# Performance work log

Measured on AMD Instinct MI355X. Metric: run time of the kernel, lower is better.

Reference implementation:

```python
import jax, jax.numpy as jnp
import numpy as np

H, W = 512, 512  # image_size from init_kwargs


def _render_single(xyz, color, opacity):
    """Faithful JAX version of GaussianRenderer._fallback_render (the path the
    module executes when the CUDA rasterizer is unavailable), vectorized.
    Point-splat each Gaussian to one pixel, depth-sort descending (back-to-front),
    alpha-composite: a_k = o_k * prod_{j<k}(1 - o_j); depth = z of front-most hit.
    xyz: (N,3)  color: (N,3)  opacity: (N,1)
    """
    N = xyz.shape[0]
    focal = (H + W) / 2.0
    z = xyz[:, 2]
    xf = xyz[:, 0] / (z + 1e-6) * focal + W / 2.0
    yf = xyz[:, 1] / (z + 1e-6) * focal + H / 2.0
    # torch .long() truncates toward zero
    xi = jnp.trunc(jnp.clip(xf, -1e9, 1e9)).astype(jnp.int32)
    yi = jnp.trunc(jnp.clip(yf, -1e9, 1e9)).astype(jnp.int32)
    valid = (xi >= 0) & (xi < W) & (yi >= 0) & (yi < H)
    pix = jnp.where(valid, yi * W + xi, H * W)  # dummy slot H*W for out-of-bounds
    # stable sort: primary pixel ascending, secondary z descending (back-to-front)
    order = jnp.lexsort((-z, pix))
    pix_s, z_s = pix[order], z[order]
    o_s = opacity[order, 0]
    c_s = color[order]
    valid_s = pix_s < H * W
    # per-pixel exclusive transmittance: alpha recurrence 1-A_k = (1-A_{k-1})(1-o_k)
    logt = jnp.log(jnp.clip(1.0 - o_s, 1e-12, None))
    cs = jnp.cumsum(logt)
    excl = cs - logt  # exclusive cumsum (global)
    start = jnp.concatenate([jnp.ones((1,), bool), pix_s[1:] != pix_s[:-1]])
    start_idx = jax.lax.cummax(jnp.where(start, jnp.arange(N), -1))
    T_prev = jnp.exp(excl - excl[start_idx])  # exclusive within pixel segment
    a = jnp.where(valid_s, o_s * T_prev, 0.0)
    img = jnp.zeros((H * W + 1, 3), xyz.dtype).at[pix_s].add(a[:, None] * c_s)
    # depth: last element written per pixel (front-most, smallest z in segment)
    end = jnp.concatenate([pix_s[1:] != pix_s[:-1], jnp.ones((1,), bool)])
    dpix = jnp.where(end & valid_s, pix_s, H * W)
    depth = jnp.zeros((H * W + 1,), xyz.dtype).at[dpix].set(z_s)
    render = img[: H * W].reshape(H, W, 3).transpose(2, 0, 1)  # (3,H,W)
    return render, depth[: H * W].reshape(1, H, W)


def setup_inputs() -> dict:
    key = jax.random.key(0)
    ks = jax.random.split(key, 5)
    B, N = 8, 262144
    return {
        "xyz": jax.random.normal(ks[0], (B, N, 3), jnp.float32),
        "scale": jax.random.normal(ks[1], (B, N, 3), jnp.float32),
        "rotation": jax.random.normal(ks[2], (B, N, 1), jnp.float32),
        "opacity": jax.random.uniform(ks[3], (B, N, 1), jnp.float32),
        "color": jax.random.uniform(ks[4], (B, N, 3), jnp.float32),
    }


def reference(xyz, scale, rotation, opacity, color):
    # scale/rotation are accepted (part of the gaussians dict) but unused by the
    # fallback renderer, matching the torch source.
    render, depth = jax.vmap(_render_single)(xyz, color, opacity)
    return render, depth
```

## Files before the change

kernel.cpp:

```cpp
#include <hip/hip_runtime.h>
#include <stdint.h>

#define W_ 512
#define H_ 512
#define HW_ (512 * 512)
#define RMAX 4
#define OVF_CAP 65536

__device__ __forceinline__ int project_pix(float x, float y, float z) {
    float zz = z + 1e-6f;
    float xf = x / zz * 512.0f + 256.0f;
    float yf = y / zz * 512.0f + 256.0f;
    xf = fminf(fmaxf(xf, -1e9f), 1e9f);
    yf = fminf(fmaxf(yf, -1e9f), 1e9f);
    int xi = (int)xf;
    int yi = (int)yf;
    if (xi >= 0 && xi < W_ && yi >= 0 && yi < H_) return yi * W_ + xi;
    return -1;
}

__device__ __forceinline__ unsigned int q8(float v) {
    v = fminf(fmaxf(v, 0.f), 1.f);
    return (unsigned int)__float2uint_rn(v * 255.0f);
}
__device__ __forceinline__ float d8(unsigned int u) {
    return (float)(u & 255u) * (1.0f / 255.0f);
}

__global__ void __launch_bounds__(256) k_init(uint4* __restrict__ p, int n4) {
    int i = blockIdx.x * blockDim.x + threadIdx.x;
    if (i < n4) p[i] = make_uint4(0u, 0u, 0u, 0u);
}

__global__ void __launch_bounds__(256) k_build(const float4* __restrict__ xyz4,
                                               const float4* __restrict__ op4,
                                               const float4* __restrict__ col4,
                                               unsigned int* __restrict__ cnt,
                                               unsigned long long* __restrict__ slots,
                                               unsigned int* __restrict__ ovf_hdr,
                                               unsigned int* __restrict__ ovf_pix,
                                               unsigned long long* __restrict__ ovf_rec,
                                               int N, int total4) {
    int t = blockIdx.x * blockDim.x + threadIdx.x;
    if (t >= total4) return;
    float4 v0 = xyz4[3 * (size_t)t + 0];
    float4 v1 = xyz4[3 * (size_t)t + 1];
    float4 v2 = xyz4[3 * (size_t)t + 2];
    float4 o4 = op4[t];
    float4 c0 = col4[3 * (size_t)t + 0];
    float4 c1 = col4[3 * (size_t)t + 1];
    float4 c2 = col4[3 * (size_t)t + 2];
    float xs[4] = {v0.x, v0.w, v1.z, v2.y};
    float ys[4] = {v0.y, v1.x, v1.w, v2.z};
    float zs[4] = {v0.z, v1.y, v2.x, v2.w};
    float os[4] = {o4.x, o4.y, o4.z, o4.w};
    float cr[4] = {c0.x, c0.w, c1.z, c2.y};
    float cg[4] = {c0.y, c1.x, c1.w, c2.z};
    float cb[4] = {c0.z, c1.y, c2.x, c2.w};
    int g0 = 4 * t;
    size_t pbase = (size_t)(g0 / N) * HW_;

    int pix[4];
    unsigned long long rec[4];
#pragma unroll
    for (int j = 0; j < 4; ++j) {
        pix[j] = project_pix(xs[j], ys[j], zs[j]);
        unsigned int pay = q8(os[j]) | (q8(cr[j]) << 8) | (q8(cg[j]) << 16) |
                           (q8(cb[j]) << 24);
        rec[j] = ((unsigned long long)__float_as_uint(zs[j]) << 32) |
                 (unsigned long long)pay;
    }

    size_t p[4];
    unsigned int sh[4], old[4];
#pragma unroll
    for (int j = 0; j < 4; ++j) {
        p[j] = pbase + (pix[j] >= 0 ? pix[j] : 0);
        sh[j] = 16u * (unsigned int)(p[j] & 1);
        if (pix[j] >= 0) old[j] = atomicAdd(&cnt[p[j] >> 1], 1u << sh[j]);
    }

#pragma unroll
    for (int j = 0; j < 4; ++j) {
        if (pix[j] >= 0) {
            unsigned int s = (old[j] >> sh[j]) & 0xffffu;
            if (s < RMAX) {
                slots[p[j] * RMAX + s] = rec[j];
            } else {
                unsigned int i = atomicAdd(ovf_hdr, 1u);
                if (i < OVF_CAP) { ovf_pix[i] = (unsigned int)p[j]; ovf_rec[i] = rec[j]; }
            }
        }
    }
}

__global__ void __launch_bounds__(256) k_composite(const unsigned int* __restrict__ cnt,
                                                   const unsigned long long* __restrict__ slots,
                                                   const unsigned int* __restrict__ ovf_hdr,
                                                   const unsigned int* __restrict__ ovf_pix,
                                                   const unsigned long long* __restrict__ ovf_rec,
                                                   float* __restrict__ out, int B) {
    int q = blockIdx.x * blockDim.x + threadIdx.x;
    int nb8 = B * (HW_ / 8);
    if (q >= nb8) return;
    int p0 = 8 * q;
    int b = p0 / HW_;
    int pl0 = p0 - b * HW_;

    uint4 cw = ((const uint4*)cnt)[q];
    unsigned int ws[4] = {cw.x, cw.y, cw.z, cw.w};

    float rr[8], gg[8], bb[8], dd[8];

#pragma unroll
    for (int j = 0; j < 8; ++j) {
        unsigned int k = (ws[j >> 1] >> (16 * (j & 1))) & 0xffffu;
        float r = 0.f, g2 = 0.f, bl = 0.f, depth = 0.f;
        if (k > 0) {
            size_t p = (size_t)p0 + j;
            const uint4* sp = (const uint4*)&slots[p * RMAX];
            uint4 s01 = sp[0];

            unsigned int pay0 = s01.x;
            float o0 = d8(pay0);
            r  = o0 * d8(pay0 >> 8);
            g2 = o0 * d8(pay0 >> 16);
            bl = o0 * d8(pay0 >> 24);
            depth = __uint_as_float(s01.y);

            if (k >= 2) {
                unsigned int pf = s01.x, pn = s01.z;
                float zf = __uint_as_float(s01.y), zn = __uint_as_float(s01.w);
                bool sw = (zn > zf) || (zn == zf && pn < pf);
                if (sw) {
                    unsigned int tp = pf; pf = pn; pn = tp;
                    float tz = zf; zf = zn; zn = tz;
                }
                float of = d8(pf), on = d8(pn);
                float a1 = on * (1.0f - of);
                r  = of * d8(pf >> 8)  + a1 * d8(pn >> 8);
                g2 = of * d8(pf >> 16) + a1 * d8(pn >> 16);
                bl = of * d8(pf >> 24) + a1 * d8(pn >> 24);
                depth = zn;

                if (k >= 3) {
                    uint4 s23 = sp[1];
                    if (k <= RMAX) {
                        float z_[4];
                        unsigned int y_[4];
                        z_[0] = __uint_as_float(s01.y); y_[0] = s01.x;
                        z_[1] = __uint_as_float(s01.w); y_[1] = s01.z;
                        z_[2] = __uint_as_float(s23.y); y_[2] = s23.x;
                        z_[3] = (k > 3) ? __uint_as_float(s23.w) : -__builtin_inff();
                        y_[3] = s23.z;
#define CE(I, J)                                                                    \
                        {                                                           \
                            bool sw2 = (z_[J] > z_[I]) || (z_[J] == z_[I] && y_[J] < y_[I]); \
                            if (sw2) {                                              \
                                float tz = z_[I]; z_[I] = z_[J]; z_[J] = tz;        \
                                unsigned int ty = y_[I]; y_[I] = y_[J]; y_[J] = ty; \
                            }                                                       \
                        }
                        CE(0,1) CE(2,3) CE(0,2) CE(1,3) CE(1,2)
#undef CE
                        float T = 1.f;
                        r = 0.f; g2 = 0.f; bl = 0.f; depth = 0.f;
#pragma unroll
                        for (int s = 0; s < RMAX; ++s) {
                            if (s < (int)k) {
                                unsigned int pay = y_[s];
                                float o = d8(pay);
                                float a = o * T;
                                r  += a * d8(pay >> 8);
                                g2 += a * d8(pay >> 16);
                                bl += a * d8(pay >> 24);
                                T *= (1.0f - o);
                                depth = z_[s];
                            }
                        }
                    } else {
                        unsigned int nov = ovf_hdr[0];
                        if (nov > OVF_CAP) nov = OVF_CAP;
                        unsigned int ptag = (unsigned int)p;
                        float zz0 = __uint_as_float(s01.y), zz1 = __uint_as_float(s01.w);
                        float zz2 = __uint_as_float(s23.y), zz3 = __uint_as_float(s23.w);
                        float prev_z = __builtin_inff();
                        unsigned int prev_y = 0u;
                        float T = 1.f;
                        r = 0.f; g2 = 0.f; bl = 0.f; depth = 0.f;
                        for (int s = 0; s < (int)k; ++s) {
                            float best_z = -__builtin_inff();
                            unsigned int best_y = ~0u;
#define CAND(Z, Y)                                                                       \
                            {                                                            \
                                float z = (Z); unsigned int y = (Y);                     \
                                bool after  = (z < prev_z) || (z == prev_z && y > prev_y); \
                                bool better = (z > best_z) || (z == best_z && y < best_y); \
                                if (after && better) { best_z = z; best_y = y; }         \
                            }
                            CAND(zz0, s01.x) CAND(zz1, s01.z) CAND(zz2, s23.x) CAND(zz3, s23.z)
                            for (unsigned int t2 = 0; t2 < nov; ++t2) {
                                if (ovf_pix[t2] == ptag) {
                                    unsigned long long rec = ovf_rec[t2];
                                    CAND(__uint_as_float((unsigned int)(rec >> 32)),
                                         (unsigned int)rec)
                                }
                            }
#undef CAND
                            unsigned int pay = best_y;
                            float o = d8(pay);
                            float a = o * T;
                            r  += a * d8(pay >> 8);
                            g2 += a * d8(pay >> 16);
                            bl += a * d8(pay >> 24);
                            T *= (1.0f - o);
                            depth = best_z;
                            prev_z = best_z;
                            prev_y = best_y;
                        }
                    }
                }
            }
        }
        rr[j] = r; gg[j] = g2; bb[j] = bl; dd[j] = depth;
    }

    size_t HWs = (size_t)HW_;
    float* oR = out + ((size_t)b * 3 + 0) * HWs + pl0;
    float* oG = out + ((size_t)b * 3 + 1) * HWs + pl0;
    float* oB = out + ((size_t)b * 3 + 2) * HWs + pl0;
    float* oD = out + (size_t)B * 3 * HWs + (size_t)b * HWs + pl0;
    *(float4*)(oR)     = make_float4(rr[0], rr[1], rr[2], rr[3]);
    *(float4*)(oR + 4) = make_float4(rr[4], rr[5], rr[6], rr[7]);
    *(float4*)(oG)     = make_float4(gg[0], gg[1], gg[2], gg[3]);
    *(float4*)(oG + 4) = make_float4(gg[4], gg[5], gg[6], gg[7]);
    *(float4*)(oB)     = make_float4(bb[0], bb[1], bb[2], bb[3]);
    *(float4*)(oB + 4) = make_float4(bb[4], bb[5], bb[6], bb[7]);
    *(float4*)(oD)     = make_float4(dd[0], dd[1], dd[2], dd[3]);
    *(float4*)(oD + 4) = make_float4(dd[4], dd[5], dd[6], dd[7]);
}

extern "C" void kernel_launch(void* const* d_in, const int* in_sizes, int n_in,
                              void* d_out, int out_size, void* d_ws, size_t ws_size,
                              hipStream_t stream) {
    const float* xyz     = (const float*)d_in[0];
    const float* opacity = (const float*)d_in[3];
    const float* color   = (const float*)d_in[4];
    float* out = (float*)d_out;

    int B = out_size / (4 * HW_);
    int N = in_sizes[0] / (3 * B);
    int total = B * N;
    int nb = B * HW_;

    unsigned int* cnt      = (unsigned int*)d_ws;
    unsigned int* ovf_hdr  = cnt + nb / 2;
    unsigned int* ovf_pix  = ovf_hdr + 64;
    unsigned long long* ovf_rec = (unsigned long long*)(ovf_pix + OVF_CAP);
    unsigned long long* slots   = ovf_rec + OVF_CAP;

    int blk = 256;
    int zwords = nb / 2 + 64;
    int z4 = zwords / 4;
    k_init<<<(z4 + blk - 1) / blk, blk, 0, stream>>>((uint4*)cnt, z4);

    int total4 = total / 4;
    k_build<<<(total4 + blk - 1) / blk, blk, 0, stream>>>((const float4*)xyz,
                                                          (const float4*)opacity,
                                                          (const float4*)color,
                                                          cnt, slots, ovf_hdr, ovf_pix, ovf_rec,
                                                          N, total4);

    int nb8 = nb / 8;
    k_composite<<<(nb8 + blk - 1) / blk, blk, 0, stream>>>(cnt, slots, ovf_hdr, ovf_pix,
                                                           ovf_rec, out, B);
}
```

Baseline: 41.71 us.

## Split per-pixel slot array into dense first-slot plane plus overflow slots

The per-pixel record storage changes from a single 4-slot array to a dense array holding each pixel's first record, plus a separate 3-slot array for the second through fourth. The composite kernel now loads the first records of 8 consecutive pixels with coalesced 16-byte loads and reads the extra slots only for pixels with two or more hits. The build kernel is also restructured to do projection, atomic, and store per point in one loop. The aim is to cut wasted memory traffic, since most pixels hold at most one splat. The cost is a less regular access pattern for multi-hit pixels and the scattered 3-wide layout.

```diff
diff --git a/kernel.cpp b/kernel.cpp
--- a/kernel.cpp
+++ b/kernel.cpp
@@ -36,7 +36,8 @@
                                                const float4* __restrict__ op4,
                                                const float4* __restrict__ col4,
                                                unsigned int* __restrict__ cnt,
-                                               unsigned long long* __restrict__ slots,
+                                               unsigned long long* __restrict__ s0,
+                                               unsigned long long* __restrict__ sx,
                                                unsigned int* __restrict__ ovf_hdr,
                                                unsigned int* __restrict__ ovf_pix,
                                                unsigned long long* __restrict__ ovf_rec,
@@ -59,43 +60,33 @@
     float cb[4] = {c0.z, c1.y, c2.x, c2.w};
     int g0 = 4 * t;
     size_t pbase = (size_t)(g0 / N) * HW_;
-
-    int pix[4];
-    unsigned long long rec[4];
 #pragma unroll
     for (int j = 0; j < 4; ++j) {
-        pix[j] = project_pix(xs[j], ys[j], zs[j]);
-        unsigned int pay = q8(os[j]) | (q8(cr[j]) << 8) | (q8(cg[j]) << 16) |
-                           (q8(cb[j]) << 24);
-        rec[j] = ((unsigned long long)__float_as_uint(zs[j]) << 32) |
-                 (unsigned long long)pay;
-    }
-
-    size_t p[4];
-    unsigned int sh[4], old[4];
-#pragma unroll
-    for (int j = 0; j < 4; ++j) {
-        p[j] = pbase + (pix[j] >= 0 ? pix[j] : 0);
-        sh[j] = 16u * (unsigned int)(p[j] & 1);
-        if (pix[j] >= 0) old[j] = atomicAdd(&cnt[p[j] >> 1], 1u << sh[j]);
-    }
-
-#pragma unroll
-    for (int j = 0; j < 4; ++j) {
-        if (pix[j] >= 0) {
-            unsigned int s = (old[j] >> sh[j]) & 0xffffu;
-            if (s < RMAX) {
-                slots[p[j] * RMAX + s] = rec[j];
+        int pix = project_pix(xs[j], ys[j], zs[j]);
+        if (pix >= 0) {
+            size_t p = pbase + pix;
+            unsigned int sh = 16u * (unsigned int)(p & 1);
+            unsigned int old = atomicAdd(&cnt[p >> 1], 1u << sh);
+            unsigned int s = (old >> sh) & 0xffffu;
+            unsigned int pay = q8(os[j]) | (q8(cr[j]) << 8) | (q8(cg[j]) << 16) |
+                               (q8(cb[j]) << 24);
+            unsigned long long rec =
+                ((unsigned long long)__float_as_uint(zs[j]) << 32) | (unsigned long long)pay;
+            if (s == 0) {
+                s0[p] = rec;
+            } else if (s < RMAX) {
+                sx[p * 3 + (s - 1)] = rec;
             } else {
                 unsigned int i = atomicAdd(ovf_hdr, 1u);
-                if (i < OVF_CAP) { ovf_pix[i] = (unsigned int)p[j]; ovf_rec[i] = rec[j]; }
+                if (i < OVF_CAP) { ovf_pix[i] = (unsigned int)p; ovf_rec[i] = rec; }
             }
         }
     }
 }
 
 __global__ void __launch_bounds__(256) k_composite(const unsigned int* __restrict__ cnt,
-                                                   const unsigned long long* __restrict__ slots,
+                                                   const unsigned long long* __restrict__ s0,
+                                                   const unsigned long long* __restrict__ sx,
                                                    const unsigned int* __restrict__ ovf_hdr,
                                                    const unsigned int* __restrict__ ovf_pix,
                                                    const unsigned long long* __restrict__ ovf_rec,
@@ -108,7 +99,12 @@
     int pl0 = p0 - b * HW_;
 
     uint4 cw = ((const uint4*)cnt)[q];
+    const uint4* s0p = (const uint4*)&s0[p0];
+    uint4 sa = s0p[0], sb = s0p[1], sc = s0p[2], sd = s0p[3];
+
     unsigned int ws[4] = {cw.x, cw.y, cw.z, cw.w};
+    unsigned int pay0_[8] = {sa.x, sa.z, sb.x, sb.z, sc.x, sc.z, sd.x, sd.z};
+    unsigned int zb0_[8]  = {sa.y, sa.w, sb.y, sb.w, sc.y, sc.w, sd.y, sd.w};
 
     float rr[8], gg[8], bb[8], dd[8];
 
@@ -118,19 +114,20 @@
         float r = 0.f, g2 = 0.f, bl = 0.f, depth = 0.f;
         if (k > 0) {
             size_t p = (size_t)p0 + j;
-            const uint4* sp = (const uint4*)&slots[p * RMAX];
-            uint4 s01 = sp[0];
-
-            unsigned int pay0 = s01.x;
-            float o0 = d8(pay0);
-            r  = o0 * d8(pay0 >> 8);
-            g2 = o0 * d8(pay0 >> 16);
-            bl = o0 * d8(pay0 >> 24);
-            depth = __uint_as_float(s01.y);
+
+            unsigned int pa = pay0_[j];
+            float o0 = d8(pa);
+            r  = o0 * d8(pa >> 8);
+            g2 = o0 * d8(pa >> 16);
+            bl = o0 * d8(pa >> 24);
+            depth = __uint_as_float(zb0_[j]);
 
             if (k >= 2) {
-                unsigned int pf = s01.x, pn = s01.z;
-                float zf = __uint_as_float(s01.y), zn = __uint_as_float(s01.w);
+                const unsigned long long* sxp = &sx[p * 3];
+                unsigned long long r1 = sxp[0];
+                unsigned int pf = pay0_[j], pn = (unsigned int)r1;
+                float zf = __uint_as_float(zb0_[j]);
+                float zn = __uint_as_float((unsigned int)(r1 >> 32));
                 bool sw = (zn > zf) || (zn == zf && pn < pf);
                 if (sw) {
                     unsigned int tp = pf; pf = pn; pn = tp;
@@ -144,15 +141,17 @@
                 depth = zn;
 
                 if (k >= 3) {
-                    uint4 s23 = sp[1];
+                    unsigned long long r2 = sxp[1];
                     if (k <= RMAX) {
+                        unsigned long long r3 = (k > 3) ? sxp[2] : 0ull;
                         float z_[4];
                         unsigned int y_[4];
-                        z_[0] = __uint_as_float(s01.y); y_[0] = s01.x;
-                        z_[1] = __uint_as_float(s01.w); y_[1] = s01.z;
-                        z_[2] = __uint_as_float(s23.y); y_[2] = s23.x;
-                        z_[3] = (k > 3) ? __uint_as_float(s23.w) : -__builtin_inff();
-                        y_[3] = s23.z;
+                        z_[0] = __uint_as_float(zb0_[j]);            y_[0] = pay0_[j];
+                        z_[1] = __uint_as_float((unsigned int)(r1 >> 32)); y_[1] = (unsigned int)r1;
+                        z_[2] = __uint_as_float((unsigned int)(r2 >> 32)); y_[2] = (unsigned int)r2;
+                        z_[3] = (k > 3) ? __uint_as_float((unsigned int)(r3 >> 32))
+                                        : -__builtin_inff();
+                        y_[3] = (unsigned int)r3;
 #define CE(I, J)                                                                    \
                         {                                                           \
                             bool sw2 = (z_[J] > z_[I]) || (z_[J] == z_[I] && y_[J] < y_[I]); \
@@ -179,11 +178,14 @@
                             }
                         }
                     } else {
+                        unsigned long long r3 = sxp[2];
                         unsigned int nov = ovf_hdr[0];
                         if (nov > OVF_CAP) nov = OVF_CAP;
                         unsigned int ptag = (unsigned int)p;
-                        float zz0 = __uint_as_float(s01.y), zz1 = __uint_as_float(s01.w);
-                        float zz2 = __uint_as_float(s23.y), zz3 = __uint_as_float(s23.w);
+                        float zz0 = __uint_as_float(zb0_[j]);
+                        float zz1 = __uint_as_float((unsigned int)(r1 >> 32));
+                        float zz2 = __uint_as_float((unsigned int)(r2 >> 32));
+                        float zz3 = __uint_as_float((unsigned int)(r3 >> 32));
                         float prev_z = __builtin_inff();
                         unsigned int prev_y = 0u;
                         float T = 1.f;
@@ -198,7 +200,8 @@
                                 bool better = (z > best_z) || (z == best_z && y < best_y); \
                                 if (after && better) { best_z = z; best_y = y; }         \
                             }
-                            CAND(zz0, s01.x) CAND(zz1, s01.z) CAND(zz2, s23.x) CAND(zz3, s23.z)
+                            CAND(zz0, pay0_[j]) CAND(zz1, (unsigned int)r1)
+                            CAND(zz2, (unsigned int)r2) CAND(zz3, (unsigned int)r3)
                             for (unsigned int t2 = 0; t2 < nov; ++t2) {
                                 if (ovf_pix[t2] == ptag) {
                                     unsigned long long rec = ovf_rec[t2];
@@ -257,7 +260,8 @@
     unsigned int* ovf_hdr  = cnt + nb / 2;
     unsigned int* ovf_pix  = ovf_hdr + 64;
     unsigned long long* ovf_rec = (unsigned long long*)(ovf_pix + OVF_CAP);
-    unsigned long long* slots   = ovf_rec + OVF_CAP;
+    unsigned long long* s0      = ovf_rec + OVF_CAP;
+    unsigned long long* sx      = s0 + nb;
 
     int blk = 256;
     int zwords = nb / 2 + 64;
@@ -268,10 +272,10 @@
     k_build<<<(total4 + blk - 1) / blk, blk, 0, stream>>>((const float4*)xyz,
                                                           (const float4*)opacity,
                                                           (const float4*)color,
-                                                          cnt, slots, ovf_hdr, ovf_pix, ovf_rec,
+                                                          cnt, s0, sx, ovf_hdr, ovf_pix, ovf_rec,
                                                           N, total4);
 
     int nb8 = nb / 8;
-    k_composite<<<(nb8 + blk - 1) / blk, blk, 0, stream>>>(cnt, slots, ovf_hdr, ovf_pix,
+    k_composite<<<(nb8 + blk - 1) / blk, blk, 0, stream>>>(cnt, s0, sx, ovf_hdr, ovf_pix,
                                                            ovf_rec, out, B);
 }
```

After: 41.10 us, median of 2. About the same (-1.5%).
